# Kernel tuning notes

Measured on AMD Instinct MI355X. Metric: run time of the kernel, lower is better.

The kernel has to match this reference:

```python
import jax, jax.numpy as jnp
import numpy as np

N = 50000
E = 800000
IN_CH = 128
HID = 32
HEADS = 8
OUT_CH = 64
NEG_SLOPE = 0.2


def _gat_layer(x, W, att_src, att_dst, bias, src, dst, H, C, concat):
    """One GATConv layer (add aggregation, self-loops appended).
    x: [n, Fin], W: [Fin, H*C], att_*: [H, C], bias: [H*C] or [C].
    src/dst: [E] int edge endpoints (no self loops; they are appended here).
    """
    n = x.shape[0]
    xs = (x @ W).reshape(n, H, C)                 # projected features [n,H,C]
    a_src = (xs * att_src).sum(-1)                # [n,H]
    a_dst = (xs * att_dst).sum(-1)                # [n,H]
    loop = jnp.arange(n, dtype=src.dtype)
    s = jnp.concatenate([src, loop])              # [E+n]
    d = jnp.concatenate([dst, loop])
    alpha = a_src[s] + a_dst[d]                   # per-edge score [E+n,H]
    alpha = jax.nn.leaky_relu(alpha, NEG_SLOPE)
    # segment softmax over destination node (every node has a self loop,
    # so no empty segments)
    amax = jax.ops.segment_max(alpha, d, num_segments=n)
    ex = jnp.exp(alpha - amax[d])
    denom = jax.ops.segment_sum(ex, d, num_segments=n)
    alpha = ex / denom[d]                         # normalized attention [E+n,H]
    # weighted scatter-add aggregation
    out = jax.ops.segment_sum(alpha[:, :, None] * xs[s], d, num_segments=n)
    out = out.reshape(n, H * C) if concat else out.mean(axis=1)
    return out + bias


def setup_inputs() -> dict:
    key = jax.random.key(0)
    ks = jax.random.split(key, 12)
    def glorot(k, shape):
        fan = shape[0] + shape[-1]
        return jax.random.uniform(k, shape, jnp.float32,
                                  -jnp.sqrt(6.0 / fan), jnp.sqrt(6.0 / fan))
    x = jax.random.normal(ks[0], (N, IN_CH), jnp.float32)
    edge_index = jax.random.randint(ks[1], (2, E), 0, N, dtype=jnp.int64)
    W1 = glorot(ks[2], (IN_CH, HEADS * HID))
    att_src1 = glorot(ks[3], (HEADS, HID))
    att_dst1 = glorot(ks[4], (HEADS, HID))
    bias1 = jnp.zeros((HEADS * HID,), jnp.float32)
    W2 = glorot(ks[5], (HEADS * HID, 1 * OUT_CH))
    att_src2 = glorot(ks[6], (1, OUT_CH))
    att_dst2 = glorot(ks[7], (1, OUT_CH))
    bias2 = jnp.zeros((OUT_CH,), jnp.float32)
    return {"x": x, "edge_index": edge_index,
            "W1": W1, "att_src1": att_src1, "att_dst1": att_dst1, "bias1": bias1,
            "W2": W2, "att_src2": att_src2, "att_dst2": att_dst2, "bias2": bias2}


def reference(x, edge_index, W1, att_src1, att_dst1, bias1,
              W2, att_src2, att_dst2, bias2):
    src, dst = edge_index[0], edge_index[1]
    h = _gat_layer(x, W1, att_src1, att_dst1, bias1, src, dst,
                   HEADS, HID, concat=True)      # [N, HEADS*HID]
    h = jax.nn.elu(h)
    out = _gat_layer(h, W2, att_src2, att_dst2, bias2, src, dst,
                     1, OUT_CH, concat=False)    # [N, OUT_CH]
    return out
```

## Files before the change

### kernel.cpp

```cpp
#include <hip/hip_runtime.h>

#define NN 50000
#define NE 800000
#define IN_CH 128
#define HID 32
#define HEADS 8
#define HC 256
#define OUT_CH 64
#define NEG_SLOPE 0.2f
#define SCAN_BLOCKS 196

typedef _Float16 half4 __attribute__((ext_vector_type(4)));
typedef _Float16 half8 __attribute__((ext_vector_type(8)));


__global__ void hist_kernel(const int* __restrict__ dst, int* __restrict__ deg) {
    int e = blockIdx.x * blockDim.x + threadIdx.x;
    if (e < NE) atomicAdd(&deg[dst[e]], 1);
}

__global__ __launch_bounds__(256)
void scan_phase1(const int* __restrict__ deg, int* __restrict__ excl,
                 int* __restrict__ bsum) {
    __shared__ int sm[256];
    const int t = blockIdx.x * 256 + threadIdx.x;
    const int v = (t < NN) ? deg[t] : 0;
    sm[threadIdx.x] = v;
    __syncthreads();
    for (int off = 1; off < 256; off <<= 1) {
        int u = (threadIdx.x >= off) ? sm[threadIdx.x - off] : 0;
        __syncthreads();
        sm[threadIdx.x] += u;
        __syncthreads();
    }
    if (t < NN) excl[t] = sm[threadIdx.x] - v;
    if (threadIdx.x == 255) bsum[blockIdx.x] = sm[255];
}

__global__ __launch_bounds__(256)
void scan_phase2(const int* __restrict__ bsum, int* __restrict__ boff,
                 int* __restrict__ offsets) {
    __shared__ int sm[256];
    const int t = threadIdx.x;
    const int v = (t < SCAN_BLOCKS) ? bsum[t] : 0;
    sm[t] = v;
    __syncthreads();
    for (int off = 1; off < 256; off <<= 1) {
        int u = (t >= off) ? sm[t - off] : 0;
        __syncthreads();
        sm[t] += u;
        __syncthreads();
    }
    if (t < SCAN_BLOCKS) boff[t] = sm[t] - v;
    if (t == 255) offsets[NN] = sm[255];
}

__global__ __launch_bounds__(256)
void scan_phase3(const int* __restrict__ excl, const int* __restrict__ boff,
                 int* __restrict__ offsets, int* __restrict__ cursor) {
    const int t = blockIdx.x * 256 + threadIdx.x;
    if (t < NN) {
        int v = excl[t] + boff[blockIdx.x];
        offsets[t] = v;
        cursor[t]  = v;
    }
}

__global__ void scatter_kernel(const int* __restrict__ src,
                               const int* __restrict__ dst,
                               int* __restrict__ cursor, int* __restrict__ ssrc) {
    int e = blockIdx.x * blockDim.x + threadIdx.x;
    if (e < NE) {
        int d = dst[e];
        int pos = atomicAdd(&cursor[d], 1);
        ssrc[pos] = src[e];
    }
}

__global__ __launch_bounds__(256)
void gemm_f32_128_h(const float* __restrict__ A, const float* __restrict__ B,
                    _Float16* __restrict__ C, int M, int N, int K) {
    __shared__ float As[16][128 + 4];
    __shared__ float Bs[16][128];
    const int tid = threadIdx.x;
    const int bm = blockIdx.x * 128;
    const int bn = blockIdx.y * 128;
    const int tx = tid & 15;
    const int ty = tid >> 4;

    float acc[8][8] = {};
    for (int k0 = 0; k0 < K; k0 += 16) {
#pragma unroll
        for (int it = 0; it < 2; ++it) {
            int idx = tid + it * 256;
            int r = idx >> 2;
            int c = (idx & 3) * 4;
            float4 av = make_float4(0.f, 0.f, 0.f, 0.f);
            int ar = bm + r;
            if (ar < M) av = *(const float4*)(A + (long)ar * K + k0 + c);
            As[c + 0][r] = av.x;
            As[c + 1][r] = av.y;
            As[c + 2][r] = av.z;
            As[c + 3][r] = av.w;
        }
#pragma unroll
        for (int it = 0; it < 2; ++it) {
            int idx = tid + it * 256;
            int r = idx >> 5;
            int c = (idx & 31) * 4;
            *(float4*)&Bs[r][c] = *(const float4*)(B + (long)(k0 + r) * N + bn + c);
        }
        __syncthreads();
#pragma unroll
        for (int kk = 0; kk < 16; ++kk) {
            float a[8], b[8];
            *(float4*)&a[0] = *(const float4*)&As[kk][ty * 4];
            *(float4*)&a[4] = *(const float4*)&As[kk][64 + ty * 4];
            *(float4*)&b[0] = *(const float4*)&Bs[kk][tx * 4];
            *(float4*)&b[4] = *(const float4*)&Bs[kk][64 + tx * 4];
#pragma unroll
            for (int i = 0; i < 8; ++i)
#pragma unroll
                for (int j = 0; j < 8; ++j) acc[i][j] += a[i] * b[j];
        }
        __syncthreads();
    }
#pragma unroll
    for (int ih = 0; ih < 2; ++ih)
#pragma unroll
    for (int i4 = 0; i4 < 4; ++i4) {
        int r = bm + ih * 64 + ty * 4 + i4;
        if (r >= M) continue;
        int i = ih * 4 + i4;
#pragma unroll
        for (int jh = 0; jh < 2; ++jh) {
            half4 hv;
            hv[0] = (_Float16)acc[i][jh * 4 + 0];
            hv[1] = (_Float16)acc[i][jh * 4 + 1];
            hv[2] = (_Float16)acc[i][jh * 4 + 2];
            hv[3] = (_Float16)acc[i][jh * 4 + 3];
            *(half4*)(C + (long)r * N + bn + jh * 64 + tx * 4) = hv;
        }
    }
}

__global__ __launch_bounds__(256)
void gemm_f32_h(const float* __restrict__ A, const float* __restrict__ B,
                _Float16* __restrict__ C, int M, int N, int K) {
    __shared__ float As[16][64 + 4];
    __shared__ float Bs[16][64];
    const int tid = threadIdx.x;
    const int bm = blockIdx.x * 64;
    const int bn = blockIdx.y * 64;
    const int tx = tid % 16;
    const int ty = tid / 16;
    const int arow = tid / 4;
    const int acol = (tid % 4) * 4;
    const int brow = tid / 16;
    const int bcol = (tid % 16) * 4;

    float acc[4][4] = {};
    for (int k0 = 0; k0 < K; k0 += 16) {
        float4 av = make_float4(0.f, 0.f, 0.f, 0.f);
        int ar = bm + arow;
        if (ar < M) av = *(const float4*)(A + (long)ar * K + k0 + acol);
        As[acol + 0][arow] = av.x;
        As[acol + 1][arow] = av.y;
        As[acol + 2][arow] = av.z;
        As[acol + 3][arow] = av.w;
        float4 bv = *(const float4*)(B + (long)(k0 + brow) * N + bn + bcol);
        *(float4*)&Bs[brow][bcol] = bv;
        __syncthreads();
#pragma unroll
        for (int kk = 0; kk < 16; ++kk) {
            float a[4], b[4];
#pragma unroll
            for (int i = 0; i < 4; ++i) a[i] = As[kk][ty * 4 + i];
#pragma unroll
            for (int j = 0; j < 4; ++j) b[j] = Bs[kk][tx * 4 + j];
#pragma unroll
            for (int i = 0; i < 4; ++i)
#pragma unroll
                for (int j = 0; j < 4; ++j) acc[i][j] += a[i] * b[j];
        }
        __syncthreads();
    }
#pragma unroll
    for (int i = 0; i < 4; ++i) {
        int r = bm + ty * 4 + i;
        if (r < M) {
            half4 hv;
            hv[0] = (_Float16)acc[i][0];
            hv[1] = (_Float16)acc[i][1];
            hv[2] = (_Float16)acc[i][2];
            hv[3] = (_Float16)acc[i][3];
            *(half4*)(C + (long)r * N + bn + tx * 4) = hv;
        }
    }
}


__global__ void attcoef1(const _Float16* __restrict__ xs, const float* __restrict__ att_s,
                         const float* __restrict__ att_d,
                         float* __restrict__ a_s, float* __restrict__ a_d) {
    int idx = blockIdx.x * blockDim.x + threadIdx.x;
    if (idx >= NN * HEADS) return;
    int h = idx & 7;
    const _Float16* xp = xs + (long)idx * 32;
    const float* sp = att_s + h * 32;
    const float* dp = att_d + h * 32;
    float as = 0.f, ad = 0.f;
#pragma unroll
    for (int i = 0; i < 4; ++i) {
        half8 v = *(const half8*)(xp + i * 8);
#pragma unroll
        for (int j = 0; j < 8; ++j) {
            float f = (float)v[j];
            as += f * sp[i * 8 + j];
            ad += f * dp[i * 8 + j];
        }
    }
    a_s[idx] = as;
    a_d[idx] = ad;
}

__global__ void attcoef2(const _Float16* __restrict__ xs, const float* __restrict__ att_s,
                         const float* __restrict__ att_d,
                         float* __restrict__ a_s, float* __restrict__ a_d) {
    int n = blockIdx.x * blockDim.x + threadIdx.x;
    if (n >= NN) return;
    const _Float16* xp = xs + (long)n * 64;
    float as = 0.f, ad = 0.f;
#pragma unroll
    for (int i = 0; i < 8; ++i) {
        half8 v = *(const half8*)(xp + i * 8);
#pragma unroll
        for (int j = 0; j < 8; ++j) {
            float f = (float)v[j];
            as += f * att_s[i * 8 + j];
            ad += f * att_d[i * 8 + j];
        }
    }
    a_s[n] = as;
    a_d[n] = ad;
}


__device__ __forceinline__ float lrelu(float x) { return x > 0.f ? x : NEG_SLOPE * x; }

__global__ __launch_bounds__(256)
void agg1(const _Float16* __restrict__ xs, const float* __restrict__ a_s,
          const float* __restrict__ a_d, const int* __restrict__ offsets,
          const int* __restrict__ ssrc, const float* __restrict__ bias,
          float* __restrict__ out) {
    __shared__ float pl_all[4][64 * 9];
    const int wslot = threadIdx.x >> 6;
    const int wave = (blockIdx.x * blockDim.x + threadIdx.x) >> 6;
    const int lane = threadIdx.x & 63;
    if (wave >= NN) return;
    float* pl = pl_all[wslot];
    const int n = wave;
    const int h = lane >> 3;
    const int ch = h * 32 + (lane & 7) * 4;

    const float4 D0 = *(const float4*)(a_d + (long)n * 8);
    const float4 D1 = *(const float4*)(a_d + (long)n * 8 + 4);
    const float adn = a_d[n * 8 + h];
    const int beg = offsets[n], end = offsets[n + 1];

    float pself = __expf(lrelu(a_s[n * 8 + h] + adn));
    float den = pself;
    float ax, ay, az, aw;
    {
        half4 v = *(const half4*)(xs + (long)n * HC + ch);
        ax = pself * (float)v[0]; ay = pself * (float)v[1];
        az = pself * (float)v[2]; aw = pself * (float)v[3];
    }

    for (int base = beg; base < end; base += 64) {
        const int cnt = min(64, end - base);
        int sidx = 0;
        if (lane < cnt) {
            sidx = ssrc[base + lane];
            const float4* ap = (const float4*)(a_s + (long)sidx * 8);
            float4 A0 = ap[0], A1 = ap[1];
            pl[lane * 9 + 0] = __expf(lrelu(A0.x + D0.x));
            pl[lane * 9 + 1] = __expf(lrelu(A0.y + D0.y));
            pl[lane * 9 + 2] = __expf(lrelu(A0.z + D0.z));
            pl[lane * 9 + 3] = __expf(lrelu(A0.w + D0.w));
            pl[lane * 9 + 4] = __expf(lrelu(A1.x + D1.x));
            pl[lane * 9 + 5] = __expf(lrelu(A1.y + D1.y));
            pl[lane * 9 + 6] = __expf(lrelu(A1.z + D1.z));
            pl[lane * 9 + 7] = __expf(lrelu(A1.w + D1.w));
        }
        asm volatile("s_waitcnt lgkmcnt(0)" ::: "memory");

        int u = 0;
        for (; u + 8 <= cnt; u += 8) {
            int s0 = __shfl(sidx, u + 0), s1 = __shfl(sidx, u + 1);
            int s2 = __shfl(sidx, u + 2), s3 = __shfl(sidx, u + 3);
            int s4 = __shfl(sidx, u + 4), s5 = __shfl(sidx, u + 5);
            int s6 = __shfl(sidx, u + 6), s7 = __shfl(sidx, u + 7);
            half4 v0 = *(const half4*)(xs + (long)s0 * HC + ch);
            half4 v1 = *(const half4*)(xs + (long)s1 * HC + ch);
            half4 v2 = *(const half4*)(xs + (long)s2 * HC + ch);
            half4 v3 = *(const half4*)(xs + (long)s3 * HC + ch);
            half4 v4 = *(const half4*)(xs + (long)s4 * HC + ch);
            half4 v5 = *(const half4*)(xs + (long)s5 * HC + ch);
            half4 v6 = *(const half4*)(xs + (long)s6 * HC + ch);
            half4 v7 = *(const half4*)(xs + (long)s7 * HC + ch);
            float p0 = pl[(u + 0) * 9 + h], p1 = pl[(u + 1) * 9 + h];
            float p2 = pl[(u + 2) * 9 + h], p3 = pl[(u + 3) * 9 + h];
            float p4 = pl[(u + 4) * 9 + h], p5 = pl[(u + 5) * 9 + h];
            float p6 = pl[(u + 6) * 9 + h], p7 = pl[(u + 7) * 9 + h];
            den += ((p0 + p1) + (p2 + p3)) + ((p4 + p5) + (p6 + p7));
            ax += p0 * (float)v0[0] + p1 * (float)v1[0] + p2 * (float)v2[0] + p3 * (float)v3[0]
                + p4 * (float)v4[0] + p5 * (float)v5[0] + p6 * (float)v6[0] + p7 * (float)v7[0];
            ay += p0 * (float)v0[1] + p1 * (float)v1[1] + p2 * (float)v2[1] + p3 * (float)v3[1]
                + p4 * (float)v4[1] + p5 * (float)v5[1] + p6 * (float)v6[1] + p7 * (float)v7[1];
            az += p0 * (float)v0[2] + p1 * (float)v1[2] + p2 * (float)v2[2] + p3 * (float)v3[2]
                + p4 * (float)v4[2] + p5 * (float)v5[2] + p6 * (float)v6[2] + p7 * (float)v7[2];
            aw += p0 * (float)v0[3] + p1 * (float)v1[3] + p2 * (float)v2[3] + p3 * (float)v3[3]
                + p4 * (float)v4[3] + p5 * (float)v5[3] + p6 * (float)v6[3] + p7 * (float)v7[3];
        }
        for (; u < cnt; ++u) {
            int s = __shfl(sidx, u);
            float p = pl[u * 9 + h];
            half4 v = *(const half4*)(xs + (long)s * HC + ch);
            den += p;
            ax += p * (float)v[0]; ay += p * (float)v[1];
            az += p * (float)v[2]; aw += p * (float)v[3];
        }
    }
    float inv = 1.0f / den;
    float4 b = *(const float4*)(bias + ch);
    float4 o;
    o.x = ax * inv + b.x; o.y = ay * inv + b.y;
    o.z = az * inv + b.z; o.w = aw * inv + b.w;
    o.x = o.x > 0.f ? o.x : expm1f(o.x);
    o.y = o.y > 0.f ? o.y : expm1f(o.y);
    o.z = o.z > 0.f ? o.z : expm1f(o.z);
    o.w = o.w > 0.f ? o.w : expm1f(o.w);
    *(float4*)(out + (long)n * HC + ch) = o;
}

__global__ __launch_bounds__(256)
void agg2(const _Float16* __restrict__ xs, const float* __restrict__ a_s,
          const float* __restrict__ a_d, const int* __restrict__ offsets,
          const int* __restrict__ ssrc, const float* __restrict__ bias,
          float* __restrict__ out) {
    const int wave = (blockIdx.x * blockDim.x + threadIdx.x) >> 6;
    const int lane = threadIdx.x & 63;
    if (wave >= NN) return;
    const int n = wave;

    const float adn = a_d[n];
    const int beg = offsets[n], end = offsets[n + 1];

    float pself = __expf(lrelu(a_s[n] + adn));
    float den = pself;
    float acc = pself * (float)xs[(long)n * OUT_CH + lane];

    for (int base = beg; base < end; base += 64) {
        const int cnt = min(64, end - base);
        int sidx = 0;
        float pe = 0.f;
        if (lane < cnt) {
            sidx = ssrc[base + lane];
            pe = __expf(lrelu(a_s[sidx] + adn));
        }
        int u = 0;
        for (; u + 8 <= cnt; u += 8) {
            int s0 = __shfl(sidx, u + 0), s1 = __shfl(sidx, u + 1);
            int s2 = __shfl(sidx, u + 2), s3 = __shfl(sidx, u + 3);
            int s4 = __shfl(sidx, u + 4), s5 = __shfl(sidx, u + 5);
            int s6 = __shfl(sidx, u + 6), s7 = __shfl(sidx, u + 7);
            float p0 = __shfl(pe, u + 0), p1 = __shfl(pe, u + 1);
            float p2 = __shfl(pe, u + 2), p3 = __shfl(pe, u + 3);
            float p4 = __shfl(pe, u + 4), p5 = __shfl(pe, u + 5);
            float p6 = __shfl(pe, u + 6), p7 = __shfl(pe, u + 7);
            float v0 = (float)xs[(long)s0 * OUT_CH + lane];
            float v1 = (float)xs[(long)s1 * OUT_CH + lane];
            float v2 = (float)xs[(long)s2 * OUT_CH + lane];
            float v3 = (float)xs[(long)s3 * OUT_CH + lane];
            float v4 = (float)xs[(long)s4 * OUT_CH + lane];
            float v5 = (float)xs[(long)s5 * OUT_CH + lane];
            float v6 = (float)xs[(long)s6 * OUT_CH + lane];
            float v7 = (float)xs[(long)s7 * OUT_CH + lane];
            den += ((p0 + p1) + (p2 + p3)) + ((p4 + p5) + (p6 + p7));
            acc += p0 * v0 + p1 * v1 + p2 * v2 + p3 * v3
                 + p4 * v4 + p5 * v5 + p6 * v6 + p7 * v7;
        }
        for (; u < cnt; ++u) {
            int s = __shfl(sidx, u);
            float p = __shfl(pe, u);
            den += p;
            acc += p * (float)xs[(long)s * OUT_CH + lane];
        }
    }
    out[(long)n * OUT_CH + lane] = acc / den + bias[lane];
}


extern "C" void kernel_launch(void* const* d_in, const int* in_sizes, int n_in,
                              void* d_out, int out_size, void* d_ws, size_t ws_size,
                              hipStream_t stream) {
    const float* x     = (const float*)d_in[0];
    const int*   ei    = (const int*)d_in[1];
    const float* W1    = (const float*)d_in[2];
    const float* atts1 = (const float*)d_in[3];
    const float* attd1 = (const float*)d_in[4];
    const float* bias1 = (const float*)d_in[5];
    const float* W2    = (const float*)d_in[6];
    const float* atts2 = (const float*)d_in[7];
    const float* attd2 = (const float*)d_in[8];
    const float* bias2 = (const float*)d_in[9];
    float*       out   = (float*)d_out;

    const int* srcp = ei;
    const int* dstp = ei + NE;

    char* ws = (char*)d_ws;
    size_t off = 0;
    auto alloc = [&](size_t bytes) -> void* {
        void* p = ws + off;
        off += (bytes + 255) & ~(size_t)255;
        return p;
    };
    _Float16* xs1h  = (_Float16*)alloc((size_t)NN * HC * 2);
    float*    h1    = (float*)alloc((size_t)NN * HC * 4);
    float*    as1   = (float*)alloc((size_t)NN * HEADS * 4);
    float*    ad1   = (float*)alloc((size_t)NN * HEADS * 4);
    int*   deg      = (int*)alloc((size_t)NN * 4);
    int*   offsets  = (int*)alloc((size_t)(NN + 1) * 4);
    int*   cursor   = (int*)alloc((size_t)NN * 4);
    int*   ssrc     = (int*)alloc((size_t)NE * 4);
    int*   excl     = (int*)alloc((size_t)NN * 4);
    int*   bsum     = (int*)alloc((size_t)SCAN_BLOCKS * 4);
    int*   boff     = (int*)alloc((size_t)SCAN_BLOCKS * 4);
    _Float16* xs2h = xs1h;
    float*    as2  = as1;
    float*    ad2  = ad1;

    hipMemsetAsync(deg, 0, (size_t)NN * 4, stream);
    hist_kernel<<<(NE + 255) / 256, 256, 0, stream>>>(dstp, deg);
    scan_phase1<<<SCAN_BLOCKS, 256, 0, stream>>>(deg, excl, bsum);
    scan_phase2<<<1, 256, 0, stream>>>(bsum, boff, offsets);
    scan_phase3<<<SCAN_BLOCKS, 256, 0, stream>>>(excl, boff, offsets, cursor);
    scatter_kernel<<<(NE + 255) / 256, 256, 0, stream>>>(srcp, dstp, cursor, ssrc);

    {
        dim3 grid((NN + 127) / 128, HC / 128);
        gemm_f32_128_h<<<grid, 256, 0, stream>>>(x, W1, xs1h, NN, HC, IN_CH);
    }
    attcoef1<<<(NN * HEADS + 255) / 256, 256, 0, stream>>>(xs1h, atts1, attd1, as1, ad1);
    agg1<<<(NN + 3) / 4, 256, 0, stream>>>(xs1h, as1, ad1, offsets, ssrc, bias1, h1);

    {
        dim3 grid((NN + 63) / 64, OUT_CH / 64);
        gemm_f32_h<<<grid, 256, 0, stream>>>(h1, W2, xs2h, NN, OUT_CH, HC);
    }
    attcoef2<<<(NN + 255) / 256, 256, 0, stream>>>(xs2h, atts2, attd2, as2, ad2);
    agg2<<<(NN + 3) / 4, 256, 0, stream>>>(xs2h, as2, ad2, offsets, ssrc, bias2, out);
}
```

Measured before the change: 381.6 us.

## Replace FP32 SIMT GEMMs with FP16 MFMA GEMMs and store h1 in half

Both projection GEMMs now run on the matrix cores through a new 64x64-tile kernel built on mfma_f32_16x16x32_f16. To feed it, x is cast to fp16 and W1/W2 are transposed and cast each call. agg1 now writes the ELU output h1 in fp16 instead of fp32, which halves that intermediate's write and read traffic. The extra cast and transpose kernels add launches and a pass over x. The fp16 inputs and h1 lower precision. The MFMA epilogue writes C with scalar fp16 stores, which may coalesce poorly.

```diff
diff --git a/kernel.cpp b/kernel.cpp
--- a/kernel.cpp
+++ b/kernel.cpp
@@ -12,6 +12,7 @@
 
 typedef _Float16 half4 __attribute__((ext_vector_type(4)));
 typedef _Float16 half8 __attribute__((ext_vector_type(8)));
+typedef float    f32x4 __attribute__((ext_vector_type(4)));
 
 
 __global__ void hist_kernel(const int* __restrict__ dst, int* __restrict__ deg) {
@@ -77,124 +78,81 @@
     }
 }
 
-__global__ __launch_bounds__(256)
-void gemm_f32_128_h(const float* __restrict__ A, const float* __restrict__ B,
-                    _Float16* __restrict__ C, int M, int N, int K) {
-    __shared__ float As[16][128 + 4];
-    __shared__ float Bs[16][128];
-    const int tid = threadIdx.x;
-    const int bm = blockIdx.x * 128;
-    const int bn = blockIdx.y * 128;
-    const int tx = tid & 15;
-    const int ty = tid >> 4;
-
-    float acc[8][8] = {};
-    for (int k0 = 0; k0 < K; k0 += 16) {
-#pragma unroll
-        for (int it = 0; it < 2; ++it) {
-            int idx = tid + it * 256;
-            int r = idx >> 2;
-            int c = (idx & 3) * 4;
-            float4 av = make_float4(0.f, 0.f, 0.f, 0.f);
-            int ar = bm + r;
-            if (ar < M) av = *(const float4*)(A + (long)ar * K + k0 + c);
-            As[c + 0][r] = av.x;
-            As[c + 1][r] = av.y;
-            As[c + 2][r] = av.z;
-            As[c + 3][r] = av.w;
-        }
-#pragma unroll
-        for (int it = 0; it < 2; ++it) {
-            int idx = tid + it * 256;
-            int r = idx >> 5;
-            int c = (idx & 31) * 4;
-            *(float4*)&Bs[r][c] = *(const float4*)(B + (long)(k0 + r) * N + bn + c);
-        }
-        __syncthreads();
-#pragma unroll
-        for (int kk = 0; kk < 16; ++kk) {
-            float a[8], b[8];
-            *(float4*)&a[0] = *(const float4*)&As[kk][ty * 4];
-            *(float4*)&a[4] = *(const float4*)&As[kk][64 + ty * 4];
-            *(float4*)&b[0] = *(const float4*)&Bs[kk][tx * 4];
-            *(float4*)&b[4] = *(const float4*)&Bs[kk][64 + tx * 4];
-#pragma unroll
-            for (int i = 0; i < 8; ++i)
-#pragma unroll
-                for (int j = 0; j < 8; ++j) acc[i][j] += a[i] * b[j];
-        }
-        __syncthreads();
-    }
-#pragma unroll
-    for (int ih = 0; ih < 2; ++ih)
-#pragma unroll
-    for (int i4 = 0; i4 < 4; ++i4) {
-        int r = bm + ih * 64 + ty * 4 + i4;
-        if (r >= M) continue;
-        int i = ih * 4 + i4;
-#pragma unroll
-        for (int jh = 0; jh < 2; ++jh) {
-            half4 hv;
-            hv[0] = (_Float16)acc[i][jh * 4 + 0];
-            hv[1] = (_Float16)acc[i][jh * 4 + 1];
-            hv[2] = (_Float16)acc[i][jh * 4 + 2];
-            hv[3] = (_Float16)acc[i][jh * 4 + 3];
-            *(half4*)(C + (long)r * N + bn + jh * 64 + tx * 4) = hv;
-        }
-    }
-}
-
-__global__ __launch_bounds__(256)
-void gemm_f32_h(const float* __restrict__ A, const float* __restrict__ B,
-                _Float16* __restrict__ C, int M, int N, int K) {
-    __shared__ float As[16][64 + 4];
-    __shared__ float Bs[16][64];
-    const int tid = threadIdx.x;
-    const int bm = blockIdx.x * 64;
-    const int bn = blockIdx.y * 64;
-    const int tx = tid % 16;
-    const int ty = tid / 16;
-    const int arow = tid / 4;
-    const int acol = (tid % 4) * 4;
-    const int brow = tid / 16;
-    const int bcol = (tid % 16) * 4;
-
-    float acc[4][4] = {};
-    for (int k0 = 0; k0 < K; k0 += 16) {
-        float4 av = make_float4(0.f, 0.f, 0.f, 0.f);
-        int ar = bm + arow;
-        if (ar < M) av = *(const float4*)(A + (long)ar * K + k0 + acol);
-        As[acol + 0][arow] = av.x;
-        As[acol + 1][arow] = av.y;
-        As[acol + 2][arow] = av.z;
-        As[acol + 3][arow] = av.w;
-        float4 bv = *(const float4*)(B + (long)(k0 + brow) * N + bn + bcol);
-        *(float4*)&Bs[brow][bcol] = bv;
-        __syncthreads();
-#pragma unroll
-        for (int kk = 0; kk < 16; ++kk) {
-            float a[4], b[4];
-#pragma unroll
-            for (int i = 0; i < 4; ++i) a[i] = As[kk][ty * 4 + i];
-#pragma unroll
-            for (int j = 0; j < 4; ++j) b[j] = Bs[kk][tx * 4 + j];
-#pragma unroll
-            for (int i = 0; i < 4; ++i)
-#pragma unroll
-                for (int j = 0; j < 4; ++j) acc[i][j] += a[i] * b[j];
-        }
-        __syncthreads();
-    }
-#pragma unroll
-    for (int i = 0; i < 4; ++i) {
-        int r = bm + ty * 4 + i;
-        if (r < M) {
-            half4 hv;
-            hv[0] = (_Float16)acc[i][0];
-            hv[1] = (_Float16)acc[i][1];
-            hv[2] = (_Float16)acc[i][2];
-            hv[3] = (_Float16)acc[i][3];
-            *(half4*)(C + (long)r * N + bn + tx * 4) = hv;
+
+__global__ void cast_f32_f16(const float* __restrict__ in, _Float16* __restrict__ out,
+                             int n8) {
+    int i = blockIdx.x * blockDim.x + threadIdx.x;
+    if (i >= n8) return;
+    float4 a = ((const float4*)in)[i * 2];
+    float4 b = ((const float4*)in)[i * 2 + 1];
+    half8 h;
+    h[0] = (_Float16)a.x; h[1] = (_Float16)a.y; h[2] = (_Float16)a.z; h[3] = (_Float16)a.w;
+    h[4] = (_Float16)b.x; h[5] = (_Float16)b.y; h[6] = (_Float16)b.z; h[7] = (_Float16)b.w;
+    ((half8*)out)[i] = h;
+}
+
+__global__ void transpose_cast(const float* __restrict__ W, _Float16* __restrict__ Wt,
+                               int K, int N) {
+    int i = blockIdx.x * blockDim.x + threadIdx.x;
+    if (i >= K * N) return;
+    int k = i / N, n = i - k * N;
+    Wt[(size_t)n * K + k] = (_Float16)W[i];
+}
+
+__global__ __launch_bounds__(256)
+void gemm_mfma_h(const _Float16* __restrict__ A, const _Float16* __restrict__ Bt,
+                 _Float16* __restrict__ C, int M, int N, int K) {
+    __shared__ _Float16 Asl[64][136];
+    __shared__ _Float16 Btl[64][136];
+    const int tid  = threadIdx.x;
+    const int wave = tid >> 6, lane = tid & 63;
+    const int lr = lane & 15, lk = lane >> 4;
+    const int bm = blockIdx.x * 64, bn = blockIdx.y * 64;
+    const int sr = tid >> 2;
+    const int ss = (tid & 3) * 32;
+
+    f32x4 acc[4];
+#pragma unroll
+    for (int i = 0; i < 4; ++i) acc[i] = (f32x4){0.f, 0.f, 0.f, 0.f};
+
+    for (int k0 = 0; k0 < K; k0 += 128) {
+        {
+            const int ar = bm + sr;
+            half8 v0 = {}, v1 = {}, v2 = {}, v3 = {};
+            if (ar < M) {
+                const half8* ga = (const half8*)(A + (size_t)ar * K + k0 + ss);
+                v0 = ga[0]; v1 = ga[1]; v2 = ga[2]; v3 = ga[3];
+            }
+            *(half8*)&Asl[sr][ss + 0]  = v0;
+            *(half8*)&Asl[sr][ss + 8]  = v1;
+            *(half8*)&Asl[sr][ss + 16] = v2;
+            *(half8*)&Asl[sr][ss + 24] = v3;
+            const half8* gb = (const half8*)(Bt + (size_t)(bn + sr) * K + k0 + ss);
+            half8 w0 = gb[0], w1 = gb[1], w2 = gb[2], w3 = gb[3];
+            *(half8*)&Btl[sr][ss + 0]  = w0;
+            *(half8*)&Btl[sr][ss + 8]  = w1;
+            *(half8*)&Btl[sr][ss + 16] = w2;
+            *(half8*)&Btl[sr][ss + 24] = w3;
+        }
+        __syncthreads();
+#pragma unroll
+        for (int kk = 0; kk < 128; kk += 32) {
+            half8 a = *(const half8*)&Asl[wave * 16 + lr][kk + lk * 8];
+#pragma unroll
+            for (int nt = 0; nt < 4; ++nt) {
+                half8 b = *(const half8*)&Btl[nt * 16 + lr][kk + lk * 8];
+                acc[nt] = __builtin_amdgcn_mfma_f32_16x16x32_f16(a, b, acc[nt], 0, 0, 0);
+            }
+        }
+        __syncthreads();
+    }
+#pragma unroll
+    for (int nt = 0; nt < 4; ++nt) {
+        const int col = bn + nt * 16 + lr;
+#pragma unroll
+        for (int r = 0; r < 4; ++r) {
+            const int m = bm + wave * 16 + lk * 4 + r;
+            if (m < M) C[(size_t)m * N + col] = (_Float16)acc[nt][r];
         }
     }
 }
@@ -252,7 +210,7 @@
 void agg1(const _Float16* __restrict__ xs, const float* __restrict__ a_s,
           const float* __restrict__ a_d, const int* __restrict__ offsets,
           const int* __restrict__ ssrc, const float* __restrict__ bias,
-          float* __restrict__ out) {
+          _Float16* __restrict__ out) {
     __shared__ float pl_all[4][64 * 9];
     const int wslot = threadIdx.x >> 6;
     const int wave = (blockIdx.x * blockDim.x + threadIdx.x) >> 6;
@@ -334,14 +292,16 @@
     }
     float inv = 1.0f / den;
     float4 b = *(const float4*)(bias + ch);
-    float4 o;
-    o.x = ax * inv + b.x; o.y = ay * inv + b.y;
-    o.z = az * inv + b.z; o.w = aw * inv + b.w;
-    o.x = o.x > 0.f ? o.x : expm1f(o.x);
-    o.y = o.y > 0.f ? o.y : expm1f(o.y);
-    o.z = o.z > 0.f ? o.z : expm1f(o.z);
-    o.w = o.w > 0.f ? o.w : expm1f(o.w);
-    *(float4*)(out + (long)n * HC + ch) = o;
+    float ox = ax * inv + b.x, oy = ay * inv + b.y;
+    float oz = az * inv + b.z, ow = aw * inv + b.w;
+    ox = ox > 0.f ? ox : expm1f(ox);
+    oy = oy > 0.f ? oy : expm1f(oy);
+    oz = oz > 0.f ? oz : expm1f(oz);
+    ow = ow > 0.f ? ow : expm1f(ow);
+    half4 ho;
+    ho[0] = (_Float16)ox; ho[1] = (_Float16)oy;
+    ho[2] = (_Float16)oz; ho[3] = (_Float16)ow;
+    *(half4*)(out + (long)n * HC + ch) = ho;
 }
 
 __global__ __launch_bounds__(256)
@@ -427,8 +387,11 @@
         off += (bytes + 255) & ~(size_t)255;
         return p;
     };
+    _Float16* xh    = (_Float16*)alloc((size_t)NN * IN_CH * 2);
     _Float16* xs1h  = (_Float16*)alloc((size_t)NN * HC * 2);
-    float*    h1    = (float*)alloc((size_t)NN * HC * 4);
+    _Float16* h1h   = (_Float16*)alloc((size_t)NN * HC * 2);
+    _Float16* W1t   = (_Float16*)alloc((size_t)HC * IN_CH * 2);
+    _Float16* W2t   = (_Float16*)alloc((size_t)OUT_CH * HC * 2);
     float*    as1   = (float*)alloc((size_t)NN * HEADS * 4);
     float*    ad1   = (float*)alloc((size_t)NN * HEADS * 4);
     int*   deg      = (int*)alloc((size_t)NN * 4);
@@ -449,16 +412,20 @@
     scan_phase3<<<SCAN_BLOCKS, 256, 0, stream>>>(excl, boff, offsets, cursor);
     scatter_kernel<<<(NE + 255) / 256, 256, 0, stream>>>(srcp, dstp, cursor, ssrc);
 
+    cast_f32_f16<<<(NN * IN_CH / 8 + 255) / 256, 256, 0, stream>>>(x, xh, NN * IN_CH / 8);
+    transpose_cast<<<(IN_CH * HC + 255) / 256, 256, 0, stream>>>(W1, W1t, IN_CH, HC);
+    transpose_cast<<<(HC * OUT_CH + 255) / 256, 256, 0, stream>>>(W2, W2t, HC, OUT_CH);
+
     {
-        dim3 grid((NN + 127) / 128, HC / 128);
-        gemm_f32_128_h<<<grid, 256, 0, stream>>>(x, W1, xs1h, NN, HC, IN_CH);
+        dim3 grid((NN + 63) / 64, HC / 64);
+        gemm_mfma_h<<<grid, 256, 0, stream>>>(xh, W1t, xs1h, NN, HC, IN_CH);
     }
     attcoef1<<<(NN * HEADS + 255) / 256, 256, 0, stream>>>(xs1h, atts1, attd1, as1, ad1);
-    agg1<<<(NN + 3) / 4, 256, 0, stream>>>(xs1h, as1, ad1, offsets, ssrc, bias1, h1);
+    agg1<<<(NN + 3) / 4, 256, 0, stream>>>(xs1h, as1, ad1, offsets, ssrc, bias1, h1h);
 
     {
         dim3 grid((NN + 63) / 64, OUT_CH / 64);
-        gemm_f32_h<<<grid, 256, 0, stream>>>(h1, W2, xs2h, NN, OUT_CH, HC);
+        gemm_mfma_h<<<grid, 256, 0, stream>>>(h1h, W2t, xs2h, NN, OUT_CH, HC);
     }
     attcoef2<<<(NN + 255) / 256, 256, 0, stream>>>(xs2h, atts2, attd2, as2, ad2);
     agg2<<<(NN + 3) / 4, 256, 0, stream>>>(xs2h, as2, ad2, offsets, ssrc, bias2, out);
```

Measured after the change: 324.9 us. -14.9%, faster.
